# Performance work log

Hardware: AMD Instinct MI355X
Metric: run time of the kernel (lower is better)

## Reference

```python
import jax, jax.numpy as jnp
import numpy as np

T, B, IN, H, L = 1024, 32, 512, 512, 2


def setup_inputs() -> dict:
    key = jax.random.key(0)
    ks = jax.random.split(key, 9)
    stdv = 1.0 / np.sqrt(H)
    u = lambda k, shape: jax.random.uniform(k, shape, jnp.float32, -stdv, stdv)
    return {
        "x": jax.random.normal(ks[0], (T, B, IN), jnp.float32),
        "w_ih0": u(ks[1], (4 * H, IN)),
        "w_hh0": u(ks[2], (4 * H, H)),
        "b_ih0": jnp.zeros((4 * H,), jnp.float32),
        "b_hh0": jnp.zeros((4 * H,), jnp.float32),
        "w_ih1": u(ks[3], (4 * H, H)),
        "w_hh1": u(ks[4], (4 * H, H)),
        "b_ih1": jnp.zeros((4 * H,), jnp.float32),
        "b_hh1": jnp.zeros((4 * H,), jnp.float32),
        "h0": jnp.zeros((L, B, H), jnp.float32),
        "c0": jnp.zeros((L, B, H), jnp.float32),
    }


def _lstm_layer(x, w_ih, b_ih, w_hh, b_hh, h0, c0):
    # Precompute input projection for the whole sequence (in2hidden), then
    # scan the strictly sequential hidden recurrence over time.
    gi = jnp.einsum("tbi,gi->tbg", x, w_ih) + b_ih  # (T, B, 4H)

    def step(carry, g):
        h, c = carry
        gates = g + h @ w_hh.T + b_hh  # (B, 4H)
        i, f, gcell, o = jnp.split(gates, 4, axis=-1)
        i = jax.nn.sigmoid(i)
        f = jax.nn.sigmoid(f)
        gcell = jnp.tanh(gcell)
        o = jax.nn.sigmoid(o)
        c = f * c + i * gcell
        h = o * jnp.tanh(c)
        return (h, c), h

    (hT, cT), hs = jax.lax.scan(step, (h0, c0), gi)
    return hs, hT, cT  # (T,B,H), (B,H), (B,H)


def reference(x, w_ih0, w_hh0, b_ih0, b_hh0, w_ih1, w_hh1, b_ih1, b_hh1, h0, c0):
    out0, h0f, c0f = _lstm_layer(x, w_ih0, b_ih0, w_hh0, b_hh0, h0[0], c0[0])
    out1, h1f, c1f = _lstm_layer(out0, w_ih1, b_ih1, w_hh1, b_hh1, h0[1], c0[1])
    h_n = jnp.stack([h0f, h1f])  # (L, B, H)
    c_n = jnp.stack([c0f, c1f])
    return out1, h_n, c_n
```

## Files before the change

### kernel.cpp

```cpp
#include <hip/hip_runtime.h>

#define TT 1024
#define BB 32
#define HH 512

typedef __attribute__((ext_vector_type(8))) __bf16 bf16x8;
typedef __attribute__((ext_vector_type(8))) short short8;
typedef __attribute__((ext_vector_type(4))) float f32x4;

union frag_u { short8 s; bf16x8 b; f32x4 f; unsigned long long q[2]; };

__device__ __forceinline__ unsigned short f2bf(float f) {
  unsigned int u = __float_as_uint(f);
  u += 0x7FFFu + ((u >> 16) & 1u);
  return (unsigned short)(u >> 16);
}

__device__ __forceinline__ bf16x8 cvt8(const float* p) {
  frag_u u;
#pragma unroll
  for (int j = 0; j < 8; ++j) u.s[j] = (short)f2bf(p[j]);
  return u.b;
}

__device__ __forceinline__ float sigm(float x) {
  return __builtin_amdgcn_rcpf(1.0f + __expf(-x));
}
__device__ __forceinline__ float tanh_(float x) {
  return 1.0f - 2.0f * __builtin_amdgcn_rcpf(1.0f + __expf(2.0f * x));
}

__device__ __forceinline__ unsigned long long aload(const unsigned long long* p) {
  return __hip_atomic_load(p, __ATOMIC_RELAXED, __HIP_MEMORY_SCOPE_AGENT);
}

__device__ __forceinline__ void poll32(const unsigned long long* q0,
                                       unsigned long long hq[32]) {
  for (int it = 0; it < (1 << 20); ++it) {
#pragma unroll
    for (int kc = 0; kc < 16; ++kc) {
      hq[2 * kc] = aload(q0 + kc * 8);
      hq[2 * kc + 1] = aload(q0 + kc * 8 + 1);
    }
    unsigned int bad = 0u;
#pragma unroll
    for (int j = 0; j < 32; ++j) {
      unsigned int lo = (unsigned int)hq[j];
      unsigned int hi = (unsigned int)(hq[j] >> 32);
      bad |= (lo == 0xFFFFFFFFu) ? 1u : 0u;
      bad |= (hi == 0xFFFFFFFFu) ? 1u : 0u;
    }
    if (__all(bad == 0u)) {
      asm volatile("" ::: "memory");
      return;
    }
  }
}

__global__ void xcvt(const float* __restrict__ x, unsigned short* __restrict__ xbf) {
  size_t i = (size_t)blockIdx.x * blockDim.x + threadIdx.x;
  const f32x4* p = (const f32x4*)x + 2 * i;
  f32x4 a = p[0], b = p[1];
  short8 o;
  o[0] = (short)f2bf(a[0]); o[1] = (short)f2bf(a[1]);
  o[2] = (short)f2bf(a[2]); o[3] = (short)f2bf(a[3]);
  o[4] = (short)f2bf(b[0]); o[5] = (short)f2bf(b[1]);
  o[6] = (short)f2bf(b[2]); o[7] = (short)f2bf(b[3]);
  *((short8*)xbf + i) = o;
}

__global__ void hfill(unsigned long long* __restrict__ a,
                      unsigned long long* __restrict__ b) {
  size_t base = (size_t)blockIdx.x * 1024 + threadIdx.x;
#pragma unroll
  for (int k = 0; k < 4; ++k) {
    size_t i = base + (size_t)k * 256;
    __hip_atomic_store(a + i, ~0ull, __ATOMIC_RELAXED, __HIP_MEMORY_SCOPE_AGENT);
    __hip_atomic_store(b + i, ~0ull, __ATOMIC_RELAXED, __HIP_MEMORY_SCOPE_AGENT);
  }
}

__global__ __launch_bounds__(64, 1) void lstm_persistent(
    const float* __restrict__ x,
    const float* __restrict__ wih0, const float* __restrict__ whh0,
    const float* __restrict__ bih0, const float* __restrict__ bhh0,
    const float* __restrict__ wih1, const float* __restrict__ whh1,
    const float* __restrict__ bih1, const float* __restrict__ bhh1,
    const float* __restrict__ h0in, const float* __restrict__ c0in,
    float* __restrict__ out,
    const unsigned short* __restrict__ xbf,
    unsigned short* __restrict__ h0buf,
    unsigned short* __restrict__ h1buf)
{
  const int lane = threadIdx.x;
  const int bid = blockIdx.x;
  const int layer = bid >> 7;
  const int sub = bid & 127;
  const int mhalf = sub & 1;
  const int slice = sub >> 1;
  const int hc0 = slice << 3;
  const int q = lane >> 4;
  const int c16 = lane & 15;
  const int cmod = lane & 7;
  const bool owner = (c16 < 8);
  const bool pstore = owner && !(c16 & 1);
  const int mbase = mhalf << 4;

  const float* wih = layer ? wih1 : wih0;
  const float* whh = layer ? whh1 : whh0;
  const float* bih = layer ? bih1 : bih0;
  const float* bhh = layer ? bhh1 : bhh0;

  const int colN0 = owner ? (hc0 + c16) : (512 + hc0 + c16 - 8);
  const int colN1 = owner ? (1024 + hc0 + c16) : (1536 + hc0 + c16 - 8);

  bf16x8 w0[32], w1[32];
#pragma unroll
  for (int kc = 0; kc < 32; ++kc) {
    const float* s0;
    const float* s1;
    if (kc < 16) {
      s0 = wih + (size_t)colN0 * HH + kc * 32 + q * 8;
      s1 = wih + (size_t)colN1 * HH + kc * 32 + q * 8;
    } else {
      s0 = whh + (size_t)colN0 * HH + (kc - 16) * 32 + q * 8;
      s1 = whh + (size_t)colN1 * HH + (kc - 16) * 32 + q * 8;
    }
    w0[kc] = cvt8(s0);
    w1[kc] = cvt8(s1);
  }
  const float bias0 = bih[colN0] + bhh[colN0];
  const float bias1 = bih[colN1] + bhh[colN1];

  float creg[4];
#pragma unroll
  for (int r = 0; r < 4; ++r) {
    int batch = mbase + q * 4 + r;
    creg[r] = c0in[(size_t)layer * BB * HH + (size_t)batch * HH + hc0 + cmod];
  }

  unsigned short* myH = layer ? h1buf : h0buf;

  {
    unsigned short* hp = myH;
#pragma unroll
    for (int r = 0; r < 4; ++r) {
      int batch = mbase + q * 4 + r;
      float hv0 = h0in[(size_t)layer * BB * HH + (size_t)batch * HH + hc0 + cmod];
      unsigned short hb = f2bf(hv0);
      unsigned int partner = (unsigned int)__shfl_xor((int)(unsigned int)hb, 1);
      unsigned int packed = ((unsigned int)hb & 0xffffu) | (partner << 16);
      if (pstore) {
        unsigned int* dst = (unsigned int*)(hp + (size_t)batch * HH + hc0 + cmod);
        __hip_atomic_store(dst, packed, __ATOMIC_RELAXED, __HIP_MEMORY_SCOPE_AGENT);
      }
    }
    asm volatile("" ::: "memory");
  }

  const size_t laneoff = (size_t)(mbase + c16) * HH + q * 8;

  for (int t = 1; t <= TT; ++t) {
    f32x4 acc0 = {bias0, bias0, bias0, bias0};
    f32x4 acc1 = {bias1, bias1, bias1, bias1};

    if (layer == 0) {
      if (xbf != nullptr) {
        const unsigned short* ip = xbf + (size_t)(t - 1) * BB * HH + laneoff;
#pragma unroll
        for (int kc = 0; kc < 16; ++kc) {
          bf16x8 a = *(const bf16x8*)(const void*)(ip + kc * 32);
          acc0 = __builtin_amdgcn_mfma_f32_16x16x32_bf16(a, w0[kc], acc0, 0, 0, 0);
          acc1 = __builtin_amdgcn_mfma_f32_16x16x32_bf16(a, w1[kc], acc1, 0, 0, 0);
        }
      } else {
        const float* ip = x + (size_t)(t - 1) * BB * HH + laneoff;
#pragma unroll
        for (int kc = 0; kc < 16; ++kc) {
          bf16x8 a = cvt8(ip + kc * 32);
          acc0 = __builtin_amdgcn_mfma_f32_16x16x32_bf16(a, w0[kc], acc0, 0, 0, 0);
          acc1 = __builtin_amdgcn_mfma_f32_16x16x32_bf16(a, w1[kc], acc1, 0, 0, 0);
        }
      }

      unsigned long long hq[32];
      poll32((const unsigned long long*)(myH + (size_t)(t - 1) * BB * HH + laneoff), hq);
#pragma unroll
      for (int kc = 0; kc < 16; ++kc) {
        frag_u u;
        u.q[0] = hq[2 * kc];
        u.q[1] = hq[2 * kc + 1];
        acc0 = __builtin_amdgcn_mfma_f32_16x16x32_bf16(u.b, w0[16 + kc], acc0, 0, 0, 0);
        acc1 = __builtin_amdgcn_mfma_f32_16x16x32_bf16(u.b, w1[16 + kc], acc1, 0, 0, 0);
      }
    } else {
      {
        unsigned long long fb[32];
        poll32((const unsigned long long*)(h1buf + (size_t)(t - 1) * BB * HH + laneoff), fb);
#pragma unroll
        for (int kc = 0; kc < 16; ++kc) {
          frag_u u;
          u.q[0] = fb[2 * kc];
          u.q[1] = fb[2 * kc + 1];
          acc0 = __builtin_amdgcn_mfma_f32_16x16x32_bf16(u.b, w0[16 + kc], acc0, 0, 0, 0);
          acc1 = __builtin_amdgcn_mfma_f32_16x16x32_bf16(u.b, w1[16 + kc], acc1, 0, 0, 0);
        }
      }
      {
        unsigned long long fa[32];
        poll32((const unsigned long long*)(h0buf + (size_t)t * BB * HH + laneoff), fa);
#pragma unroll
        for (int kc = 0; kc < 16; ++kc) {
          frag_u u;
          u.q[0] = fa[2 * kc];
          u.q[1] = fa[2 * kc + 1];
          acc0 = __builtin_amdgcn_mfma_f32_16x16x32_bf16(u.b, w0[kc], acc0, 0, 0, 0);
          acc1 = __builtin_amdgcn_mfma_f32_16x16x32_bf16(u.b, w1[kc], acc1, 0, 0, 0);
        }
      }
    }

    float hv[4];
#pragma unroll
    for (int r = 0; r < 4; ++r) {
      float a0 = acc0[r], a1 = acc1[r];
      float p0 = __shfl_xor(a0, 8);
      float p1 = __shfl_xor(a1, 8);
      float iv = owner ? a0 : p0;
      float fv = owner ? p0 : a0;
      float gv = owner ? a1 : p1;
      float ov = owner ? p1 : a1;
      iv = sigm(iv);
      fv = sigm(fv);
      gv = tanh_(gv);
      ov = sigm(ov);
      float c = fv * creg[r] + iv * gv;
      creg[r] = c;
      hv[r] = ov * tanh_(c);
    }

    {
      unsigned short* hp = myH + (size_t)t * BB * HH;
#pragma unroll
      for (int r = 0; r < 4; ++r) {
        int batch = mbase + q * 4 + r;
        unsigned short hb = f2bf(hv[r]);
        unsigned int partner = (unsigned int)__shfl_xor((int)(unsigned int)hb, 1);
        unsigned int packed = ((unsigned int)hb & 0xffffu) | (partner << 16);
        if (pstore) {
          unsigned int* dst = (unsigned int*)(hp + (size_t)batch * HH + hc0 + cmod);
          __hip_atomic_store(dst, packed, __ATOMIC_RELAXED, __HIP_MEMORY_SCOPE_AGENT);
        }
      }
      asm volatile("" ::: "memory");
    }

    if (layer) {
      float* op = out + (size_t)(t - 1) * BB * HH;
#pragma unroll
      for (int r = 0; r < 4; ++r) {
        int batch = mbase + q * 4 + r;
        if (owner) op[(size_t)batch * HH + hc0 + cmod] = hv[r];
      }
    }
    if (t == TT) {
      float* hn = out + (size_t)TT * BB * HH + (size_t)layer * BB * HH;
      float* cn = out + (size_t)TT * BB * HH + (size_t)2 * BB * HH + (size_t)layer * BB * HH;
#pragma unroll
      for (int r = 0; r < 4; ++r) {
        int batch = mbase + q * 4 + r;
        if (owner) {
          hn[(size_t)batch * HH + hc0 + cmod] = hv[r];
          cn[(size_t)batch * HH + hc0 + cmod] = creg[r];
        }
      }
    }
  }
}

extern "C" void kernel_launch(void* const* d_in, const int* in_sizes, int n_in,
                              void* d_out, int out_size, void* d_ws, size_t ws_size,
                              hipStream_t stream) {
  (void)in_sizes; (void)n_in; (void)out_size;
  const float* x = (const float*)d_in[0];
  const float* wih0 = (const float*)d_in[1];
  const float* whh0 = (const float*)d_in[2];
  const float* bih0 = (const float*)d_in[3];
  const float* bhh0 = (const float*)d_in[4];
  const float* wih1 = (const float*)d_in[5];
  const float* whh1 = (const float*)d_in[6];
  const float* bih1 = (const float*)d_in[7];
  const float* bhh1 = (const float*)d_in[8];
  const float* h0in = (const float*)d_in[9];
  const float* c0in = (const float*)d_in[10];
  float* out = (float*)d_out;
  char* ws = (char*)d_ws;

  const size_t xbf_bytes = (size_t)TT * BB * HH * 2;
  const size_t hbuf_bytes = (size_t)(TT + 1) * BB * HH * 2;
  size_t off = 4096;
  bool use_xbf = ws_size >= off + xbf_bytes + 2 * hbuf_bytes;
  unsigned short* xbf = use_xbf ? (unsigned short*)(ws + off) : nullptr;
  if (use_xbf) off += xbf_bytes;
  unsigned short* h0b = (unsigned short*)(ws + off);
  unsigned short* h1b = (unsigned short*)(ws + off + hbuf_bytes);

  hfill<<<dim3(4100), dim3(256), 0, stream>>>(
      (unsigned long long*)h0b, (unsigned long long*)h1b);
  if (use_xbf) xcvt<<<dim3(8192), dim3(256), 0, stream>>>(x, xbf);
  lstm_persistent<<<dim3(256), dim3(64), 0, stream>>>(
      x, wih0, whh0, bih0, bhh0, wih1, whh1, bih1, bhh1, h0in, c0in,
      out, xbf, h0b, h1b);
}
```

Before: 6.206 ms.

## Replace sentinel polling of hidden-state data with per-step ready flags

Instead of every wave spinning on the full 32-element bf16 hidden-state fragment until no sentinel remains, each block now publishes a per-timestep flag after draining its stores with s_waitcnt vmcnt(0). Consumers poll one flag per lane (64 producer slices) and then load the hidden state once. This cuts the sentinel-fill kernel to a small flag array and shrinks each polling load. It relies on relaxed atomics plus vmcnt draining for ordering, which risks visibility races on the data loads after the flag is seen.

After: 7.940 ms. +27.9%, slower.

```diff
diff --git a/kernel.cpp b/kernel.cpp
--- a/kernel.cpp
+++ b/kernel.cpp
@@ -3,6 +3,9 @@
 #define TT 1024
 #define BB 32
 #define HH 512
+#define SENT 0xFFFFFFFFu
+
+#define FLAG_T_STRIDE 256
 
 typedef __attribute__((ext_vector_type(8))) __bf16 bf16x8;
 typedef __attribute__((ext_vector_type(8))) short short8;
@@ -30,30 +33,32 @@
   return 1.0f - 2.0f * __builtin_amdgcn_rcpf(1.0f + __expf(2.0f * x));
 }
 
+__device__ __forceinline__ void wait_vm0() {
+  asm volatile("s_waitcnt vmcnt(0)" ::: "memory");
+}
+
 __device__ __forceinline__ unsigned long long aload(const unsigned long long* p) {
   return __hip_atomic_load(p, __ATOMIC_RELAXED, __HIP_MEMORY_SCOPE_AGENT);
 }
 
-__device__ __forceinline__ void poll32(const unsigned long long* q0,
-                                       unsigned long long hq[32]) {
-  for (int it = 0; it < (1 << 20); ++it) {
-#pragma unroll
-    for (int kc = 0; kc < 16; ++kc) {
-      hq[2 * kc] = aload(q0 + kc * 8);
-      hq[2 * kc + 1] = aload(q0 + kc * 8 + 1);
-    }
-    unsigned int bad = 0u;
-#pragma unroll
-    for (int j = 0; j < 32; ++j) {
-      unsigned int lo = (unsigned int)hq[j];
-      unsigned int hi = (unsigned int)(hq[j] >> 32);
-      bad |= (lo == 0xFFFFFFFFu) ? 1u : 0u;
-      bad |= (hi == 0xFFFFFFFFu) ? 1u : 0u;
-    }
-    if (__all(bad == 0u)) {
+__device__ __forceinline__ void probe64(const int* fp, int lane) {
+  const unsigned int* p = (const unsigned int*)fp;
+  for (int it = 0; it < (1 << 22); ++it) {
+    unsigned int v = __hip_atomic_load(p + lane, __ATOMIC_RELAXED,
+                                       __HIP_MEMORY_SCOPE_AGENT);
+    if (__all(v != SENT)) {
       asm volatile("" ::: "memory");
       return;
     }
+  }
+}
+
+__device__ __forceinline__ void load32(const unsigned long long* q0,
+                                       unsigned long long hq[32]) {
+#pragma unroll
+  for (int kc = 0; kc < 16; ++kc) {
+    hq[2 * kc] = aload(q0 + kc * 8);
+    hq[2 * kc + 1] = aload(q0 + kc * 8 + 1);
   }
 }
 
@@ -69,15 +74,9 @@
   *((short8*)xbf + i) = o;
 }
 
-__global__ void hfill(unsigned long long* __restrict__ a,
-                      unsigned long long* __restrict__ b) {
-  size_t base = (size_t)blockIdx.x * 1024 + threadIdx.x;
-#pragma unroll
-  for (int k = 0; k < 4; ++k) {
-    size_t i = base + (size_t)k * 256;
-    __hip_atomic_store(a + i, ~0ull, __ATOMIC_RELAXED, __HIP_MEMORY_SCOPE_AGENT);
-    __hip_atomic_store(b + i, ~0ull, __ATOMIC_RELAXED, __HIP_MEMORY_SCOPE_AGENT);
-  }
+__global__ void hfill(unsigned long long* __restrict__ f) {
+  size_t i = (size_t)blockIdx.x * blockDim.x + threadIdx.x;
+  __hip_atomic_store(f + i, ~0ull, __ATOMIC_RELAXED, __HIP_MEMORY_SCOPE_AGENT);
 }
 
 __global__ __launch_bounds__(64, 1) void lstm_persistent(
@@ -90,7 +89,8 @@
     float* __restrict__ out,
     const unsigned short* __restrict__ xbf,
     unsigned short* __restrict__ h0buf,
-    unsigned short* __restrict__ h1buf)
+    unsigned short* __restrict__ h1buf,
+    int* __restrict__ flags)
 {
   const int lane = threadIdx.x;
   const int bid = blockIdx.x;
@@ -141,6 +141,10 @@
 
   unsigned short* myH = layer ? h1buf : h0buf;
 
+  int* fpub = flags + (layer * 2 + mhalf) * 64 + slice;
+  const int* fprOwn = flags + (layer * 2 + mhalf) * 64;
+  const int* fprL0 = flags + FLAG_T_STRIDE + mhalf * 64;
+
   {
     unsigned short* hp = myH;
 #pragma unroll
@@ -155,8 +159,11 @@
         __hip_atomic_store(dst, packed, __ATOMIC_RELAXED, __HIP_MEMORY_SCOPE_AGENT);
       }
     }
-    asm volatile("" ::: "memory");
-  }
+  }
+  wait_vm0();
+  if (lane == 0)
+    __hip_atomic_store(fpub, 0, __ATOMIC_RELAXED, __HIP_MEMORY_SCOPE_AGENT);
+  fpub += FLAG_T_STRIDE;
 
   const size_t laneoff = (size_t)(mbase + c16) * HH + q * 8;
 
@@ -183,8 +190,10 @@
         }
       }
 
+      probe64(fprOwn, lane);
+      fprOwn += FLAG_T_STRIDE;
       unsigned long long hq[32];
-      poll32((const unsigned long long*)(myH + (size_t)(t - 1) * BB * HH + laneoff), hq);
+      load32((const unsigned long long*)(myH + (size_t)(t - 1) * BB * HH + laneoff), hq);
 #pragma unroll
       for (int kc = 0; kc < 16; ++kc) {
         frag_u u;
@@ -195,8 +204,10 @@
       }
     } else {
       {
+        probe64(fprOwn, lane);
+        fprOwn += FLAG_T_STRIDE;
         unsigned long long fb[32];
-        poll32((const unsigned long long*)(h1buf + (size_t)(t - 1) * BB * HH + laneoff), fb);
+        load32((const unsigned long long*)(h1buf + (size_t)(t - 1) * BB * HH + laneoff), fb);
 #pragma unroll
         for (int kc = 0; kc < 16; ++kc) {
           frag_u u;
@@ -207,8 +218,10 @@
         }
       }
       {
+        probe64(fprL0, lane);
+        fprL0 += FLAG_T_STRIDE;
         unsigned long long fa[32];
-        poll32((const unsigned long long*)(h0buf + (size_t)t * BB * HH + laneoff), fa);
+        load32((const unsigned long long*)(h0buf + (size_t)t * BB * HH + laneoff), fa);
 #pragma unroll
         for (int kc = 0; kc < 16; ++kc) {
           frag_u u;
@@ -252,8 +265,11 @@
           __hip_atomic_store(dst, packed, __ATOMIC_RELAXED, __HIP_MEMORY_SCOPE_AGENT);
         }
       }
-      asm volatile("" ::: "memory");
-    }
+    }
+    wait_vm0();
+    if (lane == 0)
+      __hip_atomic_store(fpub, 0, __ATOMIC_RELAXED, __HIP_MEMORY_SCOPE_AGENT);
+    fpub += FLAG_T_STRIDE;
 
     if (layer) {
       float* op = out + (size_t)(t - 1) * BB * HH;
@@ -296,19 +312,22 @@
   float* out = (float*)d_out;
   char* ws = (char*)d_ws;
 
+  const size_t flag_bytes = (size_t)(TT + 1) * FLAG_T_STRIDE * 4;
+  const size_t flag_pad = ((flag_bytes + 4095) / 4096) * 4096;
+  const size_t hbuf_bytes = (size_t)(TT + 1) * BB * HH * 2;
   const size_t xbf_bytes = (size_t)TT * BB * HH * 2;
-  const size_t hbuf_bytes = (size_t)(TT + 1) * BB * HH * 2;
-  size_t off = 4096;
-  bool use_xbf = ws_size >= off + xbf_bytes + 2 * hbuf_bytes;
-  unsigned short* xbf = use_xbf ? (unsigned short*)(ws + off) : nullptr;
-  if (use_xbf) off += xbf_bytes;
+
+  int* flags = (int*)ws;
+  size_t off = flag_pad;
   unsigned short* h0b = (unsigned short*)(ws + off);
   unsigned short* h1b = (unsigned short*)(ws + off + hbuf_bytes);
-
-  hfill<<<dim3(4100), dim3(256), 0, stream>>>(
-      (unsigned long long*)h0b, (unsigned long long*)h1b);
+  off += 2 * hbuf_bytes;
+  bool use_xbf = ws_size >= off + xbf_bytes;
+  unsigned short* xbf = use_xbf ? (unsigned short*)(ws + off) : nullptr;
+
+  hfill<<<dim3(1025), dim3(128), 0, stream>>>((unsigned long long*)ws);
   if (use_xbf) xcvt<<<dim3(8192), dim3(256), 0, stream>>>(x, xbf);
   lstm_persistent<<<dim3(256), dim3(64), 0, stream>>>(
       x, wih0, whh0, bih0, bhh0, wih1, whh1, bih1, bhh1, h0in, c0in,
-      out, xbf, h0b, h1b);
-}
+      out, xbf, h0b, h1b, flags);
+}
```

## Group four slice waves per block and share polled hidden state via LDS

Applied to the files above, without the earlier changes.

Packs four hidden-slice waves into one 256-thread block (64 blocks instead of 256). A single wave per block polls the global hidden-state buffer and broadcasts the fragments through LDS to the other waves, with block barriers in between. In layer 1, two waves poll the two input streams in parallel. This cuts the number of spinning wavefronts and the global polling traffic, at the cost of extra LDS round-trips and barriers on the per-step critical path. The workspace layout is also reordered so the h buffers come first.

Measured after the change: 6.474 ms. 1.04x slower.

```diff
diff --git a/kernel.cpp b/kernel.cpp
--- a/kernel.cpp
+++ b/kernel.cpp
@@ -28,6 +28,10 @@
 }
 __device__ __forceinline__ float tanh_(float x) {
   return 1.0f - 2.0f * __builtin_amdgcn_rcpf(1.0f + __expf(2.0f * x));
+}
+
+__device__ __forceinline__ void lgkm0() {
+  asm volatile("s_waitcnt lgkmcnt(0)" ::: "memory");
 }
 
 __device__ __forceinline__ unsigned long long aload(const unsigned long long* p) {
@@ -80,7 +84,7 @@
   }
 }
 
-__global__ __launch_bounds__(64, 1) void lstm_persistent(
+__global__ __launch_bounds__(256, 1) void lstm_persistent(
     const float* __restrict__ x,
     const float* __restrict__ wih0, const float* __restrict__ whh0,
     const float* __restrict__ bih0, const float* __restrict__ bhh0,
@@ -92,12 +96,16 @@
     unsigned short* __restrict__ h0buf,
     unsigned short* __restrict__ h1buf)
 {
-  const int lane = threadIdx.x;
+  __shared__ unsigned long long ldsA[16 * 130];
+  __shared__ unsigned long long ldsB[16 * 130];
+
+  const int tid = threadIdx.x;
+  const int lane = tid & 63;
+  const int w = tid >> 6;
   const int bid = blockIdx.x;
-  const int layer = bid >> 7;
-  const int sub = bid & 127;
-  const int mhalf = sub & 1;
-  const int slice = sub >> 1;
+  const int layer = bid >> 5;
+  const int mhalf = (bid >> 4) & 1;
+  const int slice = ((bid & 15) << 2) + w;
   const int hc0 = slice << 3;
   const int q = lane >> 4;
   const int c16 = lane & 15;
@@ -159,6 +167,7 @@
   }
 
   const size_t laneoff = (size_t)(mbase + c16) * HH + q * 8;
+  const int ldsq = c16 * 130 + q * 2;
 
   for (int t = 1; t <= TT; ++t) {
     f32x4 acc0 = {bias0, bias0, bias0, bias0};
@@ -183,39 +192,71 @@
         }
       }
 
-      unsigned long long hq[32];
-      poll32((const unsigned long long*)(myH + (size_t)(t - 1) * BB * HH + laneoff), hq);
+      if (w == 0) {
+        unsigned long long hq[32];
+        poll32((const unsigned long long*)(myH + (size_t)(t - 1) * BB * HH + laneoff), hq);
+#pragma unroll
+        for (int kc = 0; kc < 16; ++kc) {
+          frag_u u;
+          u.q[0] = hq[2 * kc];
+          u.q[1] = hq[2 * kc + 1];
+          *(f32x4*)&ldsA[ldsq + kc * 8] = u.f;
+        }
+        lgkm0();
+      }
+      __builtin_amdgcn_s_barrier();
+      frag_u fr[16];
+#pragma unroll
+      for (int kc = 0; kc < 16; ++kc) fr[kc].f = *(const f32x4*)&ldsA[ldsq + kc * 8];
+      lgkm0();
+      __builtin_amdgcn_s_barrier();
 #pragma unroll
       for (int kc = 0; kc < 16; ++kc) {
-        frag_u u;
-        u.q[0] = hq[2 * kc];
-        u.q[1] = hq[2 * kc + 1];
-        acc0 = __builtin_amdgcn_mfma_f32_16x16x32_bf16(u.b, w0[16 + kc], acc0, 0, 0, 0);
-        acc1 = __builtin_amdgcn_mfma_f32_16x16x32_bf16(u.b, w1[16 + kc], acc1, 0, 0, 0);
+        acc0 = __builtin_amdgcn_mfma_f32_16x16x32_bf16(fr[kc].b, w0[16 + kc], acc0, 0, 0, 0);
+        acc1 = __builtin_amdgcn_mfma_f32_16x16x32_bf16(fr[kc].b, w1[16 + kc], acc1, 0, 0, 0);
       }
     } else {
+      if (w == 0) {
+        unsigned long long hq[32];
+        poll32((const unsigned long long*)(h1buf + (size_t)(t - 1) * BB * HH + laneoff), hq);
+#pragma unroll
+        for (int kc = 0; kc < 16; ++kc) {
+          frag_u u;
+          u.q[0] = hq[2 * kc];
+          u.q[1] = hq[2 * kc + 1];
+          *(f32x4*)&ldsB[ldsq + kc * 8] = u.f;
+        }
+        lgkm0();
+      } else if (w == 1) {
+        unsigned long long hq[32];
+        poll32((const unsigned long long*)(h0buf + (size_t)t * BB * HH + laneoff), hq);
+#pragma unroll
+        for (int kc = 0; kc < 16; ++kc) {
+          frag_u u;
+          u.q[0] = hq[2 * kc];
+          u.q[1] = hq[2 * kc + 1];
+          *(f32x4*)&ldsA[ldsq + kc * 8] = u.f;
+        }
+        lgkm0();
+      }
+      __builtin_amdgcn_s_barrier();
       {
-        unsigned long long fb[32];
-        poll32((const unsigned long long*)(h1buf + (size_t)(t - 1) * BB * HH + laneoff), fb);
-#pragma unroll
-        for (int kc = 0; kc < 16; ++kc) {
-          frag_u u;
-          u.q[0] = fb[2 * kc];
-          u.q[1] = fb[2 * kc + 1];
-          acc0 = __builtin_amdgcn_mfma_f32_16x16x32_bf16(u.b, w0[16 + kc], acc0, 0, 0, 0);
-          acc1 = __builtin_amdgcn_mfma_f32_16x16x32_bf16(u.b, w1[16 + kc], acc1, 0, 0, 0);
-        }
-      }
-      {
-        unsigned long long fa[32];
-        poll32((const unsigned long long*)(h0buf + (size_t)t * BB * HH + laneoff), fa);
-#pragma unroll
-        for (int kc = 0; kc < 16; ++kc) {
-          frag_u u;
-          u.q[0] = fa[2 * kc];
-          u.q[1] = fa[2 * kc + 1];
-          acc0 = __builtin_amdgcn_mfma_f32_16x16x32_bf16(u.b, w0[kc], acc0, 0, 0, 0);
-          acc1 = __builtin_amdgcn_mfma_f32_16x16x32_bf16(u.b, w1[kc], acc1, 0, 0, 0);
+        frag_u fr[16];
+#pragma unroll
+        for (int kc = 0; kc < 16; ++kc) fr[kc].f = *(const f32x4*)&ldsB[ldsq + kc * 8];
+#pragma unroll
+        for (int kc = 0; kc < 16; ++kc) {
+          acc0 = __builtin_amdgcn_mfma_f32_16x16x32_bf16(fr[kc].b, w0[16 + kc], acc0, 0, 0, 0);
+          acc1 = __builtin_amdgcn_mfma_f32_16x16x32_bf16(fr[kc].b, w1[16 + kc], acc1, 0, 0, 0);
+        }
+#pragma unroll
+        for (int kc = 0; kc < 16; ++kc) fr[kc].f = *(const f32x4*)&ldsA[ldsq + kc * 8];
+        lgkm0();
+        __builtin_amdgcn_s_barrier();
+#pragma unroll
+        for (int kc = 0; kc < 16; ++kc) {
+          acc0 = __builtin_amdgcn_mfma_f32_16x16x32_bf16(fr[kc].b, w0[kc], acc0, 0, 0, 0);
+          acc1 = __builtin_amdgcn_mfma_f32_16x16x32_bf16(fr[kc].b, w1[kc], acc1, 0, 0, 0);
         }
       }
     }
@@ -296,19 +337,19 @@
   float* out = (float*)d_out;
   char* ws = (char*)d_ws;
 
+  const size_t hbuf_bytes = (size_t)(TT + 1) * BB * HH * 2;
   const size_t xbf_bytes = (size_t)TT * BB * HH * 2;
-  const size_t hbuf_bytes = (size_t)(TT + 1) * BB * HH * 2;
-  size_t off = 4096;
-  bool use_xbf = ws_size >= off + xbf_bytes + 2 * hbuf_bytes;
+
+  unsigned short* h0b = (unsigned short*)ws;
+  unsigned short* h1b = (unsigned short*)(ws + hbuf_bytes);
+  size_t off = 2 * hbuf_bytes;
+  bool use_xbf = ws_size >= off + xbf_bytes;
   unsigned short* xbf = use_xbf ? (unsigned short*)(ws + off) : nullptr;
-  if (use_xbf) off += xbf_bytes;
-  unsigned short* h0b = (unsigned short*)(ws + off);
-  unsigned short* h1b = (unsigned short*)(ws + off + hbuf_bytes);
 
   hfill<<<dim3(4100), dim3(256), 0, stream>>>(
       (unsigned long long*)h0b, (unsigned long long*)h1b);
   if (use_xbf) xcvt<<<dim3(8192), dim3(256), 0, stream>>>(x, xbf);
-  lstm_persistent<<<dim3(256), dim3(64), 0, stream>>>(
+  lstm_persistent<<<dim3(64), dim3(256), 0, stream>>>(
       x, wih0, whh0, bih0, bhh0, wih1, whh1, bih1, bhh1, h0in, c0in,
       out, xbf, h0b, h1b);
 }
```

## Rework polling with inline dwordx4 loads and XCD-aware block placement

Applied to the files above, without the earlier changes.

Replaces the atomic 64-bit polling loop with inline-asm global_load_dwordx4 bursts using cache-bypass flags, escalating to sc0 sc1 every fourth iteration. Layer-1 now issues the h0 loads early so they overlap the h1 poll and MFMAs. The grid is doubled with half the blocks exiting immediately, so the working blocks sit on a subset of XCDs via round-robin placement and share L2 for cross-block communication. This risks relying on dispatch order and on the coherence semantics of the cache flags.

Measured after the change: 8.607 ms. 1.39x slower.

```diff
diff --git a/kernel.cpp b/kernel.cpp
--- a/kernel.cpp
+++ b/kernel.cpp
@@ -8,7 +8,13 @@
 typedef __attribute__((ext_vector_type(8))) short short8;
 typedef __attribute__((ext_vector_type(4))) float f32x4;
 
-union frag_u { short8 s; bf16x8 b; f32x4 f; unsigned long long q[2]; };
+union frag_u {
+  short8 s;
+  bf16x8 b;
+  f32x4 f;
+  unsigned long long q[2];
+  unsigned int d[4];
+};
 
 __device__ __forceinline__ unsigned short f2bf(float f) {
   unsigned int u = __float_as_uint(f);
@@ -30,31 +36,46 @@
   return 1.0f - 2.0f * __builtin_amdgcn_rcpf(1.0f + __expf(2.0f * x));
 }
 
-__device__ __forceinline__ unsigned long long aload(const unsigned long long* p) {
-  return __hip_atomic_load(p, __ATOMIC_RELAXED, __HIP_MEMORY_SCOPE_AGENT);
-}
-
-__device__ __forceinline__ void poll32(const unsigned long long* q0,
-                                       unsigned long long hq[32]) {
-  for (int it = 0; it < (1 << 20); ++it) {
-#pragma unroll
-    for (int kc = 0; kc < 16; ++kc) {
-      hq[2 * kc] = aload(q0 + kc * 8);
-      hq[2 * kc + 1] = aload(q0 + kc * 8 + 1);
-    }
-    unsigned int bad = 0u;
-#pragma unroll
-    for (int j = 0; j < 32; ++j) {
-      unsigned int lo = (unsigned int)hq[j];
-      unsigned int hi = (unsigned int)(hq[j] >> 32);
-      bad |= (lo == 0xFFFFFFFFu) ? 1u : 0u;
-      bad |= (hi == 0xFFFFFFFFu) ? 1u : 0u;
-    }
-    if (__all(bad == 0u)) {
-      asm volatile("" ::: "memory");
-      return;
-    }
-  }
+#define GISSUE16(FLAGS, ADDR, FR)                                           \
+  asm volatile(                                                             \
+      "global_load_dwordx4 %0, %16, off " FLAGS "\n\t"                      \
+      "global_load_dwordx4 %1, %16, off offset:64 " FLAGS "\n\t"            \
+      "global_load_dwordx4 %2, %16, off offset:128 " FLAGS "\n\t"           \
+      "global_load_dwordx4 %3, %16, off offset:192 " FLAGS "\n\t"           \
+      "global_load_dwordx4 %4, %16, off offset:256 " FLAGS "\n\t"           \
+      "global_load_dwordx4 %5, %16, off offset:320 " FLAGS "\n\t"           \
+      "global_load_dwordx4 %6, %16, off offset:384 " FLAGS "\n\t"           \
+      "global_load_dwordx4 %7, %16, off offset:448 " FLAGS "\n\t"           \
+      "global_load_dwordx4 %8, %16, off offset:512 " FLAGS "\n\t"           \
+      "global_load_dwordx4 %9, %16, off offset:576 " FLAGS "\n\t"           \
+      "global_load_dwordx4 %10, %16, off offset:640 " FLAGS "\n\t"          \
+      "global_load_dwordx4 %11, %16, off offset:704 " FLAGS "\n\t"          \
+      "global_load_dwordx4 %12, %16, off offset:768 " FLAGS "\n\t"          \
+      "global_load_dwordx4 %13, %16, off offset:832 " FLAGS "\n\t"          \
+      "global_load_dwordx4 %14, %16, off offset:896 " FLAGS "\n\t"          \
+      "global_load_dwordx4 %15, %16, off offset:960 " FLAGS                 \
+      : "=&v"((FR)[0].f), "=&v"((FR)[1].f), "=&v"((FR)[2].f),               \
+        "=&v"((FR)[3].f), "=&v"((FR)[4].f), "=&v"((FR)[5].f),               \
+        "=&v"((FR)[6].f), "=&v"((FR)[7].f), "=&v"((FR)[8].f),               \
+        "=&v"((FR)[9].f), "=&v"((FR)[10].f), "=&v"((FR)[11].f),             \
+        "=&v"((FR)[12].f), "=&v"((FR)[13].f), "=&v"((FR)[14].f),            \
+        "=&v"((FR)[15].f)                                                   \
+      : "v"((ADDR))                                                         \
+      : "memory")
+
+#define POLLWAIT                                       \
+  do {                                                 \
+    asm volatile("s_waitcnt vmcnt(0)" ::: "memory");   \
+    __builtin_amdgcn_sched_barrier(0);                 \
+  } while (0)
+
+__device__ __forceinline__ unsigned int frbad(const frag_u fr[16]) {
+  unsigned int bad = 0u;
+#pragma unroll
+  for (int j = 0; j < 16; ++j)
+#pragma unroll
+    for (int d = 0; d < 4; ++d) bad |= (fr[j].d[d] == 0xFFFFFFFFu) ? 1u : 0u;
+  return bad;
 }
 
 __global__ void xcvt(const float* __restrict__ x, unsigned short* __restrict__ xbf) {
@@ -92,12 +113,13 @@
     unsigned short* __restrict__ h0buf,
     unsigned short* __restrict__ h1buf)
 {
+  const int bid = blockIdx.x;
+  const int c = bid & 7;
+  if (c >= 4) return;
+  const int layer = c >> 1;
+  const int mhalf = c & 1;
+  const int slice = bid >> 3;
   const int lane = threadIdx.x;
-  const int bid = blockIdx.x;
-  const int layer = bid >> 7;
-  const int sub = bid & 127;
-  const int mhalf = sub & 1;
-  const int slice = sub >> 1;
   const int hc0 = slice << 3;
   const int q = lane >> 4;
   const int c16 = lane & 15;
@@ -183,40 +205,69 @@
         }
       }
 
-      unsigned long long hq[32];
-      poll32((const unsigned long long*)(myH + (size_t)(t - 1) * BB * HH + laneoff), hq);
+      frag_u fr[16];
+      {
+        const char* p =
+            (const char*)myH + ((size_t)(t - 1) * BB * HH + laneoff) * 2;
+        int it = 0;
+        for (;;) {
+          ++it;
+          if ((it & 3) == 0) {
+            GISSUE16("sc0 sc1", p, fr);
+          } else {
+            GISSUE16("sc0", p, fr);
+          }
+          POLLWAIT;
+          if (__all(frbad(fr) == 0u)) break;
+          if (it > (1 << 20)) break;
+        }
+      }
 #pragma unroll
       for (int kc = 0; kc < 16; ++kc) {
-        frag_u u;
-        u.q[0] = hq[2 * kc];
-        u.q[1] = hq[2 * kc + 1];
-        acc0 = __builtin_amdgcn_mfma_f32_16x16x32_bf16(u.b, w0[16 + kc], acc0, 0, 0, 0);
-        acc1 = __builtin_amdgcn_mfma_f32_16x16x32_bf16(u.b, w1[16 + kc], acc1, 0, 0, 0);
+        acc0 = __builtin_amdgcn_mfma_f32_16x16x32_bf16(fr[kc].b, w0[16 + kc], acc0, 0, 0, 0);
+        acc1 = __builtin_amdgcn_mfma_f32_16x16x32_bf16(fr[kc].b, w1[16 + kc], acc1, 0, 0, 0);
       }
     } else {
+      frag_u fa[16], fb[16];
+      const char* pa =
+          (const char*)h0buf + ((size_t)t * BB * HH + laneoff) * 2;
+      GISSUE16("sc0 sc1", pa, fa);
+
       {
-        unsigned long long fb[32];
-        poll32((const unsigned long long*)(h1buf + (size_t)(t - 1) * BB * HH + laneoff), fb);
-#pragma unroll
-        for (int kc = 0; kc < 16; ++kc) {
-          frag_u u;
-          u.q[0] = fb[2 * kc];
-          u.q[1] = fb[2 * kc + 1];
-          acc0 = __builtin_amdgcn_mfma_f32_16x16x32_bf16(u.b, w0[16 + kc], acc0, 0, 0, 0);
-          acc1 = __builtin_amdgcn_mfma_f32_16x16x32_bf16(u.b, w1[16 + kc], acc1, 0, 0, 0);
-        }
-      }
-      {
-        unsigned long long fa[32];
-        poll32((const unsigned long long*)(h0buf + (size_t)t * BB * HH + laneoff), fa);
-#pragma unroll
-        for (int kc = 0; kc < 16; ++kc) {
-          frag_u u;
-          u.q[0] = fa[2 * kc];
-          u.q[1] = fa[2 * kc + 1];
-          acc0 = __builtin_amdgcn_mfma_f32_16x16x32_bf16(u.b, w0[kc], acc0, 0, 0, 0);
-          acc1 = __builtin_amdgcn_mfma_f32_16x16x32_bf16(u.b, w1[kc], acc1, 0, 0, 0);
-        }
+        const char* p =
+            (const char*)h1buf + ((size_t)(t - 1) * BB * HH + laneoff) * 2;
+        int it = 0;
+        for (;;) {
+          ++it;
+          if ((it & 3) == 0) {
+            GISSUE16("sc0 sc1", p, fb);
+          } else {
+            GISSUE16("sc0", p, fb);
+          }
+          POLLWAIT;
+          if (__all(frbad(fb) == 0u)) break;
+          if (it > (1 << 20)) break;
+        }
+      }
+#pragma unroll
+      for (int kc = 0; kc < 16; ++kc) {
+        acc0 = __builtin_amdgcn_mfma_f32_16x16x32_bf16(fb[kc].b, w0[16 + kc], acc0, 0, 0, 0);
+        acc1 = __builtin_amdgcn_mfma_f32_16x16x32_bf16(fb[kc].b, w1[16 + kc], acc1, 0, 0, 0);
+      }
+      if (!__all(frbad(fa) == 0u)) {
+        int it = 0;
+        for (;;) {
+          ++it;
+          GISSUE16("sc0 sc1", pa, fa);
+          POLLWAIT;
+          if (__all(frbad(fa) == 0u)) break;
+          if (it > (1 << 20)) break;
+        }
+      }
+#pragma unroll
+      for (int kc = 0; kc < 16; ++kc) {
+        acc0 = __builtin_amdgcn_mfma_f32_16x16x32_bf16(fa[kc].b, w0[kc], acc0, 0, 0, 0);
+        acc1 = __builtin_amdgcn_mfma_f32_16x16x32_bf16(fa[kc].b, w1[kc], acc1, 0, 0, 0);
       }
     }
 
@@ -234,9 +285,9 @@
       fv = sigm(fv);
       gv = tanh_(gv);
       ov = sigm(ov);
-      float c = fv * creg[r] + iv * gv;
-      creg[r] = c;
-      hv[r] = ov * tanh_(c);
+      float cc = fv * creg[r] + iv * gv;
+      creg[r] = cc;
+      hv[r] = ov * tanh_(cc);
     }
 
     {
@@ -296,19 +347,19 @@
   float* out = (float*)d_out;
   char* ws = (char*)d_ws;
 
+  const size_t hbuf_bytes = (size_t)(TT + 1) * BB * HH * 2;
   const size_t xbf_bytes = (size_t)TT * BB * HH * 2;
-  const size_t hbuf_bytes = (size_t)(TT + 1) * BB * HH * 2;
-  size_t off = 4096;
-  bool use_xbf = ws_size >= off + xbf_bytes + 2 * hbuf_bytes;
+
+  unsigned short* h0b = (unsigned short*)ws;
+  unsigned short* h1b = (unsigned short*)(ws + hbuf_bytes);
+  size_t off = 2 * hbuf_bytes;
+  bool use_xbf = ws_size >= off + xbf_bytes;
   unsigned short* xbf = use_xbf ? (unsigned short*)(ws + off) : nullptr;
-  if (use_xbf) off += xbf_bytes;
-  unsigned short* h0b = (unsigned short*)(ws + off);
-  unsigned short* h1b = (unsigned short*)(ws + off + hbuf_bytes);
 
   hfill<<<dim3(4100), dim3(256), 0, stream>>>(
       (unsigned long long*)h0b, (unsigned long long*)h1b);
   if (use_xbf) xcvt<<<dim3(8192), dim3(256), 0, stream>>>(x, xbf);
-  lstm_persistent<<<dim3(256), dim3(64), 0, stream>>>(
+  lstm_persistent<<<dim3(512), dim3(64), 0, stream>>>(
       x, wih0, whh0, bih0, bhh0, wih1, whh1, bih1, bhh1, h0in, c0in,
       out, xbf, h0b, h1b);
 }
```
